# Kernel optimization log

Measured on AMD Instinct MI355X. Metric: run time of the kernel, lower is better.

## Reference

```python
import jax, jax.numpy as jnp
import numpy as np
from jax import lax

B, C, H, W = 4, 256, 64, 64
M = 8
CP = C // M  # 32 attention channels
KS = (3, 5, 7, 9)
EPS = 1e-5


def conv1x1(a, w, b):
    # a: [B,Ci,H,W], w: [Co,Ci], b: [Co]
    return jnp.einsum('bchw,oc->bohw', a, w) + b[None, :, None, None]


def _patches(a, k):
    # im2col with padding k//2, stride 1 (matches torch.nn.Unfold(k,1,k//2,1))
    pad = k // 2
    p = lax.conv_general_dilated_patches(a, (k, k), (1, 1), [(pad, pad), (pad, pad)])
    Bb, Cc = a.shape[0], a.shape[1]
    return p.reshape(Bb, Cc, k * k, a.shape[2], a.shape[3])  # [B,C',k^2,H,W]


def local_attn(km, qm, xm, k):
    # query is the center of each patch == qm itself (stride 1, pad k//2)
    kp = _patches(km, k)                                   # [B,C',k^2,H,W]
    scores = jnp.einsum('bckhw,bchw->bkhw', kp, qm)        # per-pixel k^2 logits
    attn = jax.nn.softmax(scores, axis=1)                  # softmax over window (dim=-2 in torch)
    xp = _patches(xm, k)                                   # [B,C',k^2,H,W]
    return jnp.einsum('bckhw,bkhw->bchw', xp, attn)        # [B,C',H,W]


def setup_inputs() -> dict:
    key = jax.random.key(0)
    ks = jax.random.split(key, 12)
    s_in = 1.0 / np.sqrt(C)
    s_out = 1.0 / np.sqrt(CP)
    return {
        'x': jax.random.normal(ks[0], (B, C, H, W), jnp.float32),
        'vessel': jax.random.uniform(ks[1], (B, 1, H, W), jnp.float32),
        'wk': jax.random.normal(ks[2], (CP, C), jnp.float32) * s_in,
        'bk': jnp.zeros((CP,), jnp.float32),
        'wq': jax.random.normal(ks[3], (CP, C), jnp.float32) * s_in,
        'bq': jnp.zeros((CP,), jnp.float32),
        'wx': jax.random.normal(ks[4], (CP, C), jnp.float32) * s_in,
        'bx': jnp.zeros((CP,), jnp.float32),
        'wf': jax.random.normal(ks[5], (C, CP), jnp.float32) * s_out,
        'bf': jnp.zeros((C,), jnp.float32),
        'gamma': jnp.ones((C,), jnp.float32),
        'beta': jnp.zeros((C,), jnp.float32),
    }


def reference(x, vessel, wk, bk, wq, bq, wx, bx, wf, bf, gamma, beta):
    km = conv1x1(x, wk, bk) * vessel   # key map masked by vessel
    qm = conv1x1(x, wq, bq)            # query map
    xm = conv1x1(x, wx, bx)            # value map
    pre = local_attn(km, qm, xm, KS[0])
    for k in KS[1:]:
        pre = pre + local_attn(km, qm, xm, k)
    y = conv1x1(pre, wf, bf)           # [B,C,H,W]
    # BatchNorm2d (training-mode batch stats)
    mean = y.mean(axis=(0, 2, 3), keepdims=True)
    var = y.var(axis=(0, 2, 3), keepdims=True)
    yn = (y - mean) * lax.rsqrt(var + EPS)
    return x + gamma[None, :, None, None] * yn + beta[None, :, None, None]
```

## Files before the change

kernel.cpp:

```cpp
#include <hip/hip_runtime.h>
#include <hip/hip_bf16.h>

typedef __hip_bfloat16 bf16;
typedef unsigned short u16;
typedef unsigned int u32;

typedef __bf16 bf16x8 __attribute__((ext_vector_type(8)));
typedef float f32x4 __attribute__((ext_vector_type(4)));

__device__ __forceinline__ float bf2f(bf16 v) { return __bfloat162float(v); }
__device__ __forceinline__ float us2f(u16 u) {
    union { u32 i; float f; } c; c.i = ((u32)u) << 16; return c.f;
}
__device__ __forceinline__ u16 f2u(float f) {
    union { bf16 b; u16 u; } c; c.b = __float2bfloat16(f); return c.u;
}

__global__ __launch_bounds__(256) void k_proj(
    const float* __restrict__ x, const float* __restrict__ vessel,
    const float* __restrict__ wk, const float* __restrict__ bk,
    const float* __restrict__ wq, const float* __restrict__ bq,
    const float* __restrict__ wx, const float* __restrict__ bx,
    bf16* __restrict__ km, bf16* __restrict__ qm, bf16* __restrict__ xm,
    float* __restrict__ partials)
{
    __shared__ u16 xs[64 * 264];
    __shared__ u16 wsh[48 * 264];
    const int tid = threadIdx.x;
    const int bid = blockIdx.x;
    const int nh = bid & 1;
    const int pt = bid >> 1;
    const int b  = pt >> 6;
    const int p0 = (pt & 63) * 64;

    if (bid < 64) {
#pragma unroll
        for (int i = 0; i < 5; ++i) {
            const int idx = tid + i * 256;
            if (idx < 1056) partials[bid * 1056 + idx] = 0.f;
        }
    }

#pragma unroll
    for (int i = 0; i < 16; ++i) {
        const int idx4 = tid + i * 256;
        const int ch = idx4 >> 4;
        const int px4 = (idx4 & 15) * 4;
        const float4 v = *(const float4*)&x[(b * 256 + ch) * 4096 + p0 + px4];
        xs[(px4 + 0) * 264 + ch] = f2u(v.x);
        xs[(px4 + 1) * 264 + ch] = f2u(v.y);
        xs[(px4 + 2) * 264 + ch] = f2u(v.z);
        xs[(px4 + 3) * 264 + ch] = f2u(v.w);
    }
#pragma unroll
    for (int i = 0; i < 12; ++i) {
        const int idx4 = tid + i * 256;
        const int o = idx4 >> 6;
        const int ch4 = (idx4 & 63) * 4;
        const int go = nh * 48 + o;
        const float* wp = (go < 32) ? wk : ((go < 64) ? wq : wx);
        const float4 v = *(const float4*)&wp[(go & 31) * 256 + ch4];
        wsh[o * 264 + ch4 + 0] = f2u(v.x);
        wsh[o * 264 + ch4 + 1] = f2u(v.y);
        wsh[o * 264 + ch4 + 2] = f2u(v.z);
        wsh[o * 264 + ch4 + 3] = f2u(v.w);
    }
    __syncthreads();

    const int w = tid >> 6;
    const int lane = tid & 63;
    const int lm = lane & 15, quad = lane >> 4;

    f32x4 acc0 = {0.f, 0.f, 0.f, 0.f};
    f32x4 acc1 = {0.f, 0.f, 0.f, 0.f};
    f32x4 acc2 = {0.f, 0.f, 0.f, 0.f};
#pragma unroll
    for (int kk = 0; kk < 8; ++kk) {
        const int k0 = kk * 32 + quad * 8;
        const bf16x8 a  = *(const bf16x8*)&xs[(w * 16 + lm) * 264 + k0];
        const bf16x8 b0 = *(const bf16x8*)&wsh[(0 + lm) * 264 + k0];
        const bf16x8 b1 = *(const bf16x8*)&wsh[(16 + lm) * 264 + k0];
        const bf16x8 b2 = *(const bf16x8*)&wsh[(32 + lm) * 264 + k0];
        acc0 = __builtin_amdgcn_mfma_f32_16x16x32_bf16(a, b0, acc0, 0, 0, 0);
        acc1 = __builtin_amdgcn_mfma_f32_16x16x32_bf16(a, b1, acc1, 0, 0, 0);
        acc2 = __builtin_amdgcn_mfma_f32_16x16x32_bf16(a, b2, acc2, 0, 0, 0);
    }
#pragma unroll
    for (int t = 0; t < 3; ++t) {
        const f32x4 acc = (t == 0) ? acc0 : ((t == 1) ? acc1 : acc2);
        const int go = nh * 48 + t * 16 + lm;
        const float* bs = (go < 32) ? bk : ((go < 64) ? bq : bx);
        const float bias = bs[go & 31];
        bf16* dst = (go < 32) ? km : ((go < 64) ? qm : xm);
#pragma unroll
        for (int rg = 0; rg < 4; ++rg) {
            const int px = p0 + w * 16 + quad * 4 + rg;
            float vv = acc[rg] + bias;
            if (go < 32) vv *= vessel[b * 4096 + px];
            dst[(b * 4096 + px) * 32 + (go & 31)] = __float2bfloat16(vv);
        }
    }
}

__global__ __launch_bounds__(256, 3) void k_attn(
    const bf16* __restrict__ km, const bf16* __restrict__ qm,
    const bf16* __restrict__ xm, bf16* __restrict__ pre,
    float* __restrict__ partials)
{
    __shared__ u16 kT[192 * 40];
    __shared__ u16 xTt[32 * 200];
    __shared__ float S[32 * 196];
    u16* P = kT;
    u16* preT = (u16*)S;

    const int tid = threadIdx.x;
    const int b = blockIdx.x >> 7;
    const int t128 = blockIdx.x & 127;
    const int h0 = (t128 >> 3) * 4;
    const int w0 = (t128 & 7) * 8;
    const u16* uk = (const u16*)km;
    const u16* ux = (const u16*)xm;
    const u16* uq = (const u16*)qm;
    const uint4 z4 = {0u, 0u, 0u, 0u};

#pragma unroll
    for (int i = 0; i < 3; ++i) {
        const int idx4 = tid + i * 256;
        const int pos = idx4 >> 2, c8 = idx4 & 3;
        const int gh = h0 - 4 + (pos >> 4), gw = w0 - 4 + (pos & 15);
        uint4 kv = z4, xv = z4;
        if (gh >= 0 && gh < 64 && gw >= 0 && gw < 64) {
            const int g = ((b << 12) + (gh << 6) + gw) * 32 + c8 * 8;
            kv = *(const uint4*)&uk[g];
            xv = *(const uint4*)&ux[g];
        }
        *(uint4*)&kT[pos * 40 + c8 * 8] = kv;
        const u16* xu = (const u16*)&xv;
#pragma unroll
        for (int t = 0; t < 8; ++t)
            xTt[(c8 * 8 + t) * 200 + pos] = xu[t];
    }
    __syncthreads();

    const int w = tid >> 6;
    const int lane = tid & 63;
    const int lm = lane & 15, quad = lane >> 4;

#pragma unroll
    for (int i = 0; i < 6; ++i) {
        const int t = w + i * 4;
        const int m = t / 12, n = t - m * 12;
        const int am = m * 16 + lm;
        const int qgh = h0 + (am >> 3), qgw = w0 + (am & 7);
        const bf16x8 a =
            *(const bf16x8*)&uq[(((b << 12) + (qgh << 6) + qgw) << 5) + quad * 8];
        const bf16x8 bb = *(const bf16x8*)&kT[(n * 16 + lm) * 40 + quad * 8];
        f32x4 acc = {0.f, 0.f, 0.f, 0.f};
        acc = __builtin_amdgcn_mfma_f32_16x16x32_bf16(a, bb, acc, 0, 0, 0);
#pragma unroll
        for (int rg = 0; rg < 4; ++rg)
            S[(m * 16 + quad * 4 + rg) * 196 + n * 16 + lm] = acc[rg];
    }
    __syncthreads();

    const int px = tid >> 3, cg = tid & 7;
    const int ty = px >> 3, tx = px & 7;
    float e[24];
    float Z3 = 0.f, Z5 = 0.f, Z7 = 0.f, Z9 = 0.f;
#pragma unroll
    for (int i = 0; i < 24; ++i) {
        const int pos = cg + 8 * i;
        const int hy = pos >> 4, hx = pos & 15;
        const int dy = hy - 4 - ty, dx = hx - 4 - tx;
        const int ady = dy < 0 ? -dy : dy, adx = dx < 0 ? -dx : dx;
        const int r = ady > adx ? ady : adx;
        const float s = S[px * 196 + pos];
        const float ev = (r <= 4) ? __expf(s) : 0.f;
        e[i] = ev;
        if (r <= 1) Z3 += ev;
        if (r <= 2) Z5 += ev;
        if (r <= 3) Z7 += ev;
        Z9 += ev;
    }
#pragma unroll
    for (int m = 1; m <= 4; m <<= 1) {
        Z3 += __shfl_xor(Z3, m);
        Z5 += __shfl_xor(Z5, m);
        Z7 += __shfl_xor(Z7, m);
        Z9 += __shfl_xor(Z9, m);
    }
    const float iZ3 = 1.f / Z3, iZ5 = 1.f / Z5, iZ7 = 1.f / Z7, iZ9 = 1.f / Z9;
#pragma unroll
    for (int i = 0; i < 24; ++i) {
        const int pos = cg + 8 * i;
        const int hy = pos >> 4, hx = pos & 15;
        const int dy = hy - 4 - ty, dx = hx - 4 - tx;
        const int ady = dy < 0 ? -dy : dy, adx = dx < 0 ? -dx : dx;
        const int r = ady > adx ? ady : adx;
        float coef = iZ9;
        if (r <= 1) coef += iZ3;
        if (r <= 2) coef += iZ5;
        if (r <= 3) coef += iZ7;
        P[px * 200 + pos] = f2u(e[i] * coef);
    }
    __syncthreads();

    const int m0 = w >> 1, n0 = w & 1;
    f32x4 acc = {0.f, 0.f, 0.f, 0.f};
#pragma unroll
    for (int kk = 0; kk < 6; ++kk) {
        const int k0 = kk * 32 + quad * 8;
        const bf16x8 a = *(const bf16x8*)&P[(m0 * 16 + lm) * 200 + k0];
        const bf16x8 bb = *(const bf16x8*)&xTt[(n0 * 16 + lm) * 200 + k0];
        acc = __builtin_amdgcn_mfma_f32_16x16x32_bf16(a, bb, acc, 0, 0, 0);
    }
#pragma unroll
    for (int rg = 0; rg < 4; ++rg) {
        const int pl = m0 * 16 + quad * 4 + rg;
        const int gh = h0 + (pl >> 3), gw = w0 + (pl & 7);
        pre[(((b << 12) + (gh << 6) + gw) << 5) + n0 * 16 + lm] =
            __float2bfloat16(acc[rg]);
        preT[(n0 * 16 + lm) * 40 + pl] = f2u(acc[rg]);
    }
    __syncthreads();

    const int it = w >> 1, jt = w & 1;
    if (w != 2) {
        const bf16x8 ca = *(const bf16x8*)&preT[(it * 16 + lm) * 40 + quad * 8];
        const bf16x8 cb = *(const bf16x8*)&preT[(jt * 16 + lm) * 40 + quad * 8];
        f32x4 cacc = {0.f, 0.f, 0.f, 0.f};
        cacc = __builtin_amdgcn_mfma_f32_16x16x32_bf16(ca, cb, cacc, 0, 0, 0);
        float* pslot = &partials[(blockIdx.x & 63) * 1056];
#pragma unroll
        for (int rg = 0; rg < 4; ++rg) {
            const int ii = it * 16 + quad * 4 + rg, jj = jt * 16 + lm;
            atomicAdd(&pslot[ii * 32 + jj], cacc[rg]);
        }
    }
    if (tid < 128) {
        float* pslot = &partials[(blockIdx.x & 63) * 1056];
        const int cc = tid >> 2, sg = tid & 3;
        float s = 0.f;
#pragma unroll
        for (int p = 0; p < 8; ++p) s += us2f(preT[cc * 40 + sg * 8 + p]);
        s += __shfl_xor(s, 1);
        s += __shfl_xor(s, 2);
        if (sg == 0) atomicAdd(&pslot[1024 + cc], s);
    }
}

__global__ __launch_bounds__(256) void k_out(
    const bf16* __restrict__ pre, const float* __restrict__ wf,
    const float* __restrict__ partials, const float* __restrict__ gamma,
    const float* __restrict__ beta, const float* __restrict__ x,
    float* __restrict__ out)
{
    __shared__ u16 wh[256 * 40];
    __shared__ u16 wl[256 * 40];
    __shared__ u16 pL[32 * 40];
    __shared__ float cov[1024];
    __shared__ float mu[32];
    __shared__ float As[256];
    __shared__ float Ss[256];
    const int tid = threadIdx.x;
    const int gp0 = blockIdx.x * 32;
    const int b = gp0 >> 12, p0 = gp0 & 4095;

#pragma unroll
    for (int i = 0; i < 8; ++i) {
        const int idx = tid + i * 256;
        const int o = idx >> 3, c4 = idx & 7;
        const float4 v = *(const float4*)&wf[o * 32 + c4 * 4];
        ushort4 hv, lv;
        hv.x = f2u(v.x); lv.x = f2u(v.x - us2f(hv.x));
        hv.y = f2u(v.y); lv.y = f2u(v.y - us2f(hv.y));
        hv.z = f2u(v.z); lv.z = f2u(v.z - us2f(hv.z));
        hv.w = f2u(v.w); lv.w = f2u(v.w - us2f(hv.w));
        *(ushort4*)&wh[o * 40 + c4 * 4] = hv;
        *(ushort4*)&wl[o * 40 + c4 * 4] = lv;
    }
    if (tid < 128) {
        const int px = tid >> 2, c8 = tid & 3;
        *(uint4*)&pL[px * 40 + c8 * 8] =
            *(const uint4*)&((const u16*)pre)[(gp0 + px) * 32 + c8 * 8];
    }
    {
        float4 a4 = {0.f, 0.f, 0.f, 0.f};
        for (int blk = 0; blk < 64; ++blk) {
            const float4 p = *(const float4*)&partials[blk * 1056 + tid * 4];
            a4.x += p.x; a4.y += p.y; a4.z += p.z; a4.w += p.w;
        }
        *(float4*)&cov[tid * 4] = a4;
    }
    if (tid < 32) {
        float s = 0.f;
        for (int blk = 0; blk < 64; ++blk) s += partials[blk * 1056 + 1024 + tid];
        mu[tid] = s * (1.f / 16384.f);
    }
    __syncthreads();

    {
        const int fi = 16 + (tid >> 4), fj = tid & 15;
        cov[fi * 32 + fj] = cov[fj * 32 + fi];
    }
    __syncthreads();

    {
        float wo[32];
#pragma unroll
        for (int c8 = 0; c8 < 4; ++c8) {
            const uint4 hv = *(const uint4*)&wh[tid * 40 + c8 * 8];
            const uint4 lv = *(const uint4*)&wl[tid * 40 + c8 * 8];
            const u16* hp = (const u16*)&hv;
            const u16* lp = (const u16*)&lv;
#pragma unroll
            for (int t = 0; t < 8; ++t)
                wo[c8 * 8 + t] = us2f(hp[t]) + us2f(lp[t]);
        }
        float mv = 0.f;
#pragma unroll
        for (int c = 0; c < 32; ++c) mv += wo[c] * mu[c];
        float qacc = 0.f;
        for (int i2 = 0; i2 < 32; ++i2) {
            float t = 0.f;
#pragma unroll
            for (int j2 = 0; j2 < 32; ++j2) t += wo[j2] * cov[i2 * 32 + j2];
            qacc += wo[i2] * t;
        }
        const float var = qacc * (1.f / 16384.f) - mv * mv;
        const float A = gamma[tid] * rsqrtf(var + 1e-5f);
        As[tid] = A;
        Ss[tid] = beta[tid] - A * mv;
    }
    __syncthreads();

    const int w = tid >> 6;
    const int lane = tid & 63;
    const int lm = lane & 15, quad = lane >> 4;

    bf16x8 pb[2];
    pb[0] = *(const bf16x8*)&pL[(0 + lm) * 40 + quad * 8];
    pb[1] = *(const bf16x8*)&pL[(16 + lm) * 40 + quad * 8];

    f32x4 acc[4][2];
#pragma unroll
    for (int mm = 0; mm < 4; ++mm) {
        const int orow = w * 64 + mm * 16 + lm;
        const bf16x8 ah = *(const bf16x8*)&wh[orow * 40 + quad * 8];
        const bf16x8 al = *(const bf16x8*)&wl[orow * 40 + quad * 8];
#pragma unroll
        for (int n = 0; n < 2; ++n) {
            f32x4 t = {0.f, 0.f, 0.f, 0.f};
            t = __builtin_amdgcn_mfma_f32_16x16x32_bf16(ah, pb[n], t, 0, 0, 0);
            acc[mm][n] =
                __builtin_amdgcn_mfma_f32_16x16x32_bf16(al, pb[n], t, 0, 0, 0);
        }
    }

#pragma unroll
    for (int mm = 0; mm < 4; ++mm) {
#pragma unroll
        for (int rg = 0; rg < 4; ++rg) {
            const int o = w * 64 + mm * 16 + quad * 4 + rg;
            const float Ao = As[o], So = Ss[o];
#pragma unroll
            for (int n = 0; n < 2; ++n) {
                const int ga = ((b << 8) + o) * 4096 + p0 + n * 16 + lm;
                out[ga] = x[ga] + Ao * acc[mm][n][rg] + So;
            }
        }
    }
}

extern "C" void kernel_launch(void* const* d_in, const int* in_sizes, int n_in,
                              void* d_out, int out_size, void* d_ws, size_t ws_size,
                              hipStream_t stream)
{
    (void)in_sizes; (void)n_in; (void)out_size; (void)ws_size;
    float* out = (float*)d_out;
    char* ws = (char*)d_ws;

    const float* x      = (const float*)d_in[0];
    const float* vessel = (const float*)d_in[1];
    const float* wk     = (const float*)d_in[2];
    const float* bk     = (const float*)d_in[3];
    const float* wq     = (const float*)d_in[4];
    const float* bq     = (const float*)d_in[5];
    const float* wx     = (const float*)d_in[6];
    const float* bx     = (const float*)d_in[7];
    const float* wf     = (const float*)d_in[8];
    const float* gamma  = (const float*)d_in[10];
    const float* beta   = (const float*)d_in[11];

    bf16* km  = (bf16*)(ws);
    bf16* qm  = (bf16*)(ws + 1048576);
    bf16* xm  = (bf16*)(ws + 2097152);
    bf16* pre = (bf16*)(ws + 3145728);
    float* partials = (float*)(ws + 4194304);

    k_proj <<<512, 256, 0, stream>>>(x, vessel, wk, bk, wq, bq, wx, bx,
                                     km, qm, xm, partials);
    k_attn <<<512, 256, 0, stream>>>(km, qm, xm, pre, partials);
    k_out  <<<512, 256, 0, stream>>>(pre, wf, partials, gamma, beta, x, out);
}
```

Measured before the change: 120.2 us.

## Alias attention LDS buffers to cut footprint and raise k_attn occupancy

Shrinks k_attn shared memory by aliasing the key and value-transposed tiles, and placing P and preT inside the score buffer. The value tile is held in registers and transposed into LDS only after the score MFMAs, behind an extra barrier. Query fragments are loaded once before the first barrier instead of inside the MFMA loop. Softmax reads and P writes become contiguous vectorized 16-byte accesses per thread, and launch bounds move to four blocks per SIMD. This targets latency hiding and LDS instruction count, at the cost of more live registers, one more sync, and possible bank conflicts from the new contiguous-per-thread pattern.

```diff
diff --git a/kernel.cpp b/kernel.cpp
--- a/kernel.cpp
+++ b/kernel.cpp
@@ -102,16 +102,18 @@
     }
 }
 
-__global__ __launch_bounds__(256, 3) void k_attn(
+__global__ __launch_bounds__(256, 4) void k_attn(
     const bf16* __restrict__ km, const bf16* __restrict__ qm,
     const bf16* __restrict__ xm, bf16* __restrict__ pre,
     float* __restrict__ partials)
 {
-    __shared__ u16 kT[192 * 40];
-    __shared__ u16 xTt[32 * 200];
-    __shared__ float S[32 * 196];
-    u16* P = kT;
-    u16* preT = (u16*)S;
+    __shared__ u16 A1[192 * 40];
+    __shared__ float A2f[32 * 196];
+    u16* kT  = A1;
+    u16* xTt = A1;
+    float* S = A2f;
+    u16* P    = (u16*)A2f;
+    u16* preT = (u16*)A2f + 6400;
 
     const int tid = threadIdx.x;
     const int b = blockIdx.x >> 7;
@@ -123,40 +125,41 @@
     const u16* uq = (const u16*)qm;
     const uint4 z4 = {0u, 0u, 0u, 0u};
 
+    const int w = tid >> 6;
+    const int lane = tid & 63;
+    const int lm = lane & 15, quad = lane >> 4;
+
+    uint4 xv[3];
 #pragma unroll
     for (int i = 0; i < 3; ++i) {
         const int idx4 = tid + i * 256;
         const int pos = idx4 >> 2, c8 = idx4 & 3;
         const int gh = h0 - 4 + (pos >> 4), gw = w0 - 4 + (pos & 15);
-        uint4 kv = z4, xv = z4;
+        uint4 kv = z4;
+        xv[i] = z4;
         if (gh >= 0 && gh < 64 && gw >= 0 && gw < 64) {
             const int g = ((b << 12) + (gh << 6) + gw) * 32 + c8 * 8;
             kv = *(const uint4*)&uk[g];
-            xv = *(const uint4*)&ux[g];
+            xv[i] = *(const uint4*)&ux[g];
         }
         *(uint4*)&kT[pos * 40 + c8 * 8] = kv;
-        const u16* xu = (const u16*)&xv;
-#pragma unroll
-        for (int t = 0; t < 8; ++t)
-            xTt[(c8 * 8 + t) * 200 + pos] = xu[t];
-    }
-    __syncthreads();
-
-    const int w = tid >> 6;
-    const int lane = tid & 63;
-    const int lm = lane & 15, quad = lane >> 4;
+    }
+    bf16x8 qa[2];
+#pragma unroll
+    for (int m = 0; m < 2; ++m) {
+        const int am = m * 16 + lm;
+        const int qgh = h0 + (am >> 3), qgw = w0 + (am & 7);
+        qa[m] = *(const bf16x8*)&uq[(((b << 12) + (qgh << 6) + qgw) << 5) + quad * 8];
+    }
+    __syncthreads();
 
 #pragma unroll
     for (int i = 0; i < 6; ++i) {
         const int t = w + i * 4;
         const int m = t / 12, n = t - m * 12;
-        const int am = m * 16 + lm;
-        const int qgh = h0 + (am >> 3), qgw = w0 + (am & 7);
-        const bf16x8 a =
-            *(const bf16x8*)&uq[(((b << 12) + (qgh << 6) + qgw) << 5) + quad * 8];
         const bf16x8 bb = *(const bf16x8*)&kT[(n * 16 + lm) * 40 + quad * 8];
         f32x4 acc = {0.f, 0.f, 0.f, 0.f};
-        acc = __builtin_amdgcn_mfma_f32_16x16x32_bf16(a, bb, acc, 0, 0, 0);
+        acc = __builtin_amdgcn_mfma_f32_16x16x32_bf16(qa[m], bb, acc, 0, 0, 0);
 #pragma unroll
         for (int rg = 0; rg < 4; ++rg)
             S[(m * 16 + quad * 4 + rg) * 196 + n * 16 + lm] = acc[rg];
@@ -168,19 +171,32 @@
     float e[24];
     float Z3 = 0.f, Z5 = 0.f, Z7 = 0.f, Z9 = 0.f;
 #pragma unroll
-    for (int i = 0; i < 24; ++i) {
-        const int pos = cg + 8 * i;
-        const int hy = pos >> 4, hx = pos & 15;
-        const int dy = hy - 4 - ty, dx = hx - 4 - tx;
-        const int ady = dy < 0 ? -dy : dy, adx = dx < 0 ? -dx : dx;
-        const int r = ady > adx ? ady : adx;
-        const float s = S[px * 196 + pos];
-        const float ev = (r <= 4) ? __expf(s) : 0.f;
-        e[i] = ev;
-        if (r <= 1) Z3 += ev;
-        if (r <= 2) Z5 += ev;
-        if (r <= 3) Z7 += ev;
-        Z9 += ev;
+    for (int i4 = 0; i4 < 6; ++i4) {
+        const f32x4 sv = *(const f32x4*)&S[px * 196 + cg * 24 + i4 * 4];
+#pragma unroll
+        for (int k = 0; k < 4; ++k) {
+            const int j = i4 * 4 + k;
+            const int pos = cg * 24 + j;
+            const int hy = pos >> 4, hx = pos & 15;
+            const int dy = hy - 4 - ty, dx = hx - 4 - tx;
+            const int ady = dy < 0 ? -dy : dy, adx = dx < 0 ? -dx : dx;
+            const int r = ady > adx ? ady : adx;
+            const float ev = (r <= 4) ? __expf(sv[k]) : 0.f;
+            e[j] = ev;
+            if (r <= 1) Z3 += ev;
+            if (r <= 2) Z5 += ev;
+            if (r <= 3) Z7 += ev;
+            Z9 += ev;
+        }
+    }
+#pragma unroll
+    for (int i = 0; i < 3; ++i) {
+        const int idx4 = tid + i * 256;
+        const int pos = idx4 >> 2, c8 = idx4 & 3;
+        const u16* xu = (const u16*)&xv[i];
+#pragma unroll
+        for (int t = 0; t < 8; ++t)
+            xTt[(c8 * 8 + t) * 200 + pos] = xu[t];
     }
 #pragma unroll
     for (int m = 1; m <= 4; m <<= 1) {
@@ -189,10 +205,13 @@
         Z7 += __shfl_xor(Z7, m);
         Z9 += __shfl_xor(Z9, m);
     }
+    __syncthreads();
+
     const float iZ3 = 1.f / Z3, iZ5 = 1.f / Z5, iZ7 = 1.f / Z7, iZ9 = 1.f / Z9;
-#pragma unroll
-    for (int i = 0; i < 24; ++i) {
-        const int pos = cg + 8 * i;
+    __attribute__((aligned(16))) u16 pw[24];
+#pragma unroll
+    for (int j = 0; j < 24; ++j) {
+        const int pos = cg * 24 + j;
         const int hy = pos >> 4, hx = pos & 15;
         const int dy = hy - 4 - ty, dx = hx - 4 - tx;
         const int ady = dy < 0 ? -dy : dy, adx = dx < 0 ? -dx : dx;
@@ -201,8 +220,11 @@
         if (r <= 1) coef += iZ3;
         if (r <= 2) coef += iZ5;
         if (r <= 3) coef += iZ7;
-        P[px * 200 + pos] = f2u(e[i] * coef);
-    }
+        pw[j] = f2u(e[j] * coef);
+    }
+#pragma unroll
+    for (int v = 0; v < 3; ++v)
+        *(uint4*)&P[px * 200 + cg * 24 + v * 8] = *(const uint4*)&pw[v * 8];
     __syncthreads();
 
     const int m0 = w >> 1, n0 = w & 1;
@@ -240,9 +262,11 @@
     if (tid < 128) {
         float* pslot = &partials[(blockIdx.x & 63) * 1056];
         const int cc = tid >> 2, sg = tid & 3;
+        const uint4 pv = *(const uint4*)&preT[cc * 40 + sg * 8];
+        const u16* pp = (const u16*)&pv;
         float s = 0.f;
 #pragma unroll
-        for (int p = 0; p < 8; ++p) s += us2f(preT[cc * 40 + sg * 8 + p]);
+        for (int p = 0; p < 8; ++p) s += us2f(pp[p]);
         s += __shfl_xor(s, 1);
         s += __shfl_xor(s, 2);
         if (sg == 0) atomicAdd(&pslot[1024 + cc], s);
```

Result: slower. 124.7 us (+3.7%).
